# Kernel optimization log

Measured on AMD Instinct MI355X. Metric: run time of the kernel, lower is better.

Reference implementation:

```python
import jax, jax.numpy as jnp
import numpy as np

B, L, D = 4, 512, 768
NUM_SPANS = 4096
MAX_WIDTH = 8
DFF = 4 * D


def setup_inputs() -> dict:
    key = jax.random.key(0)
    k_h, k_s, k_w, k1, k2 = jax.random.split(key, 5)
    h = jax.random.normal(k_h, (B, L, D), dtype=jnp.float32)
    starts = jax.random.randint(k_s, (B, NUM_SPANS), 0, L)
    widths = jax.random.randint(k_w, (B, NUM_SPANS), 1, MAX_WIDTH + 1)
    ends = jnp.minimum(starts + widths - 1, L - 1)
    span_idx = jnp.stack([starts, ends], axis=-1).astype(jnp.int64 if jax.config.jax_enable_x64 else jnp.int32)
    W1 = jax.random.normal(k1, (D, DFF), dtype=jnp.float32) * (1.0 / np.sqrt(D))
    b1 = jnp.zeros((DFF,), dtype=jnp.float32)
    W2 = jax.random.normal(k2, (DFF, D), dtype=jnp.float32) * (1.0 / np.sqrt(DFF))
    b2 = jnp.zeros((D,), dtype=jnp.float32)
    return {"h": h, "span_idx": span_idx, "W1": W1, "b1": b1, "W2": W2, "b2": b2,
            "max_width": MAX_WIDTH}


def reference(h, span_idx, W1, b1, W2, b2, max_width):
    # h: [B, L, D]; span_idx: [B, S, 2] (start, end inclusive)
    Bv, Lv, Dv = h.shape
    starts = span_idx[:, :, 0]                       # [B, S]
    lengths = span_idx[:, :, 1] - starts + 1         # [B, S]
    offsets = jnp.arange(max_width)                  # static bound on span length
    positions = starts[:, :, None] + offsets[None, None, :]      # [B, S, W]
    mask = offsets[None, None, :] < lengths[:, :, None]          # [B, S, W]
    positions = jnp.clip(positions * mask, 0, Lv - 1)
    # indexed gather-reduce (no [B,S,L,D] broadcast): [B, S, W, D]
    gathered = h[jnp.arange(Bv)[:, None, None], positions]
    summed = jnp.sum(gathered * mask[..., None].astype(h.dtype), axis=2)  # [B, S, D]
    span_reps = summed / lengths[..., None].astype(h.dtype)
    # projection: Linear -> ReLU -> (Dropout: identity at eval) -> Linear
    hmid = jax.nn.relu(jnp.einsum('bsd,df->bsf', span_reps, W1) + b1)
    out = jnp.einsum('bsf,fd->bsd', hmid, W2) + b2
    return out
```

## Files before the change

### kernel.cpp

```cpp
#include <hip/hip_runtime.h>
#include <stdint.h>

#define B_DIM 4
#define L_DIM 512
#define D_DIM 768
#define S_DIM 4096
#define DFF_DIM 3072
#define M_DIM (B_DIM * S_DIM)

typedef unsigned short ushort_t;
typedef __attribute__((ext_vector_type(8))) short short8;
typedef __attribute__((ext_vector_type(4))) float floatx4;

__device__ __forceinline__ ushort_t f2bf(float x) {
  unsigned int u = __float_as_uint(x);
  u += 0x7FFFu + ((u >> 16) & 1u);
  return (ushort_t)(u >> 16);
}

__device__ __forceinline__ void load_lds16(const ushort_t* g, ushort_t* lds) {
  __builtin_amdgcn_global_load_lds(
      (const __attribute__((address_space(1))) unsigned int*)g,
      (__attribute__((address_space(3))) unsigned int*)lds, 16, 0, 0);
}

__global__ __launch_bounds__(256)
void transpose_bf16(const float* __restrict__ in, ushort_t* __restrict__ out,
                    int K, int N) {
  __shared__ float tile[32][33];
  const int k0 = blockIdx.x * 32;
  const int n0 = blockIdx.y * 32;
  const int tx = threadIdx.x & 31;
  const int ty = threadIdx.x >> 5;
#pragma unroll
  for (int r = 0; r < 32; r += 8)
    tile[ty + r][tx] = in[(long)(k0 + ty + r) * N + n0 + tx];
  __syncthreads();
#pragma unroll
  for (int r = 0; r < 32; r += 8)
    out[(long)(n0 + ty + r) * K + k0 + tx] = f2bf(tile[tx][ty + r]);
}

__global__ __launch_bounds__(256)
void span_reps(const float* __restrict__ h, const int* __restrict__ span_idx,
               ushort_t* __restrict__ A) {
  const int span = blockIdx.x;
  const int b = span >> 12;
  const int tid = threadIdx.x;
  const int start = span_idx[span * 2 + 0];
  const int end   = span_idx[span * 2 + 1];
  const float inv = 1.0f / (float)(end - start + 1);
  const float* hb = h + ((long)b * L_DIM + start) * D_DIM;
  float a0 = 0.f, a1 = 0.f, a2 = 0.f;
  for (int p = start; p <= end; ++p) {
    a0 += hb[tid];
    a1 += hb[tid + 256];
    a2 += hb[tid + 512];
    hb += D_DIM;
  }
  ushort_t* o = A + (long)span * D_DIM;
  o[tid]       = f2bf(a0 * inv);
  o[tid + 256] = f2bf(a1 * inv);
  o[tid + 512] = f2bf(a2 * inv);
}

template <int MODE>
__global__ __launch_bounds__(256)
void gemm_bt(const ushort_t* __restrict__ A, const ushort_t* __restrict__ Bt,
             const float* __restrict__ bias, void* __restrict__ Cv,
             int M, int N, int K) {
  __shared__ ushort_t As[128 * 32];
  __shared__ ushort_t Bs[128 * 32];

  const int tid  = threadIdx.x;
  const int lane = tid & 63;
  const int wave = tid >> 6;
  const int l16  = lane & 15;
  const int quad = lane >> 4;

  const int bm = blockIdx.x;
  const int bn = blockIdx.y;

  const int wm = (wave & 1) * 64;
  const int wn = (wave >> 1) * 64;

  floatx4 acc[4][4];
#pragma unroll
  for (int i = 0; i < 4; ++i)
#pragma unroll
    for (int j = 0; j < 4; ++j)
      acc[i][j] = (floatx4)0.0f;

  const int s0 = tid, s1 = tid + 256;
  const ushort_t* gA0 = A + (long)(bm * 128 + (s0 >> 2)) * K + (s0 & 3) * 8;
  const ushort_t* gA1 = A + (long)(bm * 128 + (s1 >> 2)) * K + (s1 & 3) * 8;
  const ushort_t* gB0 = Bt + (long)(bn * 128 + (s0 >> 2)) * K + (s0 & 3) * 8;
  const ushort_t* gB1 = Bt + (long)(bn * 128 + (s1 >> 2)) * K + (s1 & 3) * 8;
  ushort_t* lA0 = As + s0 * 8;
  ushort_t* lA1 = As + s1 * 8;
  ushort_t* lB0 = Bs + s0 * 8;
  ushort_t* lB1 = Bs + s1 * 8;

  for (int k0 = 0; k0 < K; k0 += 32) {
    load_lds16(gA0, lA0);
    load_lds16(gA1, lA1);
    load_lds16(gB0, lB0);
    load_lds16(gB1, lB1);
    gA0 += 32; gA1 += 32; gB0 += 32; gB1 += 32;
    __syncthreads();

    short8 af[4], bf[4];
#pragma unroll
    for (int i = 0; i < 4; ++i)
      af[i] = *(const short8*)(As + (wm + i * 16 + l16) * 32 + quad * 8);
#pragma unroll
    for (int j = 0; j < 4; ++j)
      bf[j] = *(const short8*)(Bs + (wn + j * 16 + l16) * 32 + quad * 8);
#pragma unroll
    for (int i = 0; i < 4; ++i)
#pragma unroll
      for (int j = 0; j < 4; ++j)
        acc[i][j] = __builtin_amdgcn_mfma_f32_16x16x32_bf16(af[i], bf[j], acc[i][j], 0, 0, 0);
    __syncthreads();
  }

#pragma unroll
  for (int i = 0; i < 4; ++i) {
#pragma unroll
    for (int j = 0; j < 4; ++j) {
      const int col = bn * 128 + wn + j * 16 + l16;
      const float bv = bias[col];
      const int row0 = bm * 128 + wm + i * 16 + quad * 4;
#pragma unroll
      for (int r = 0; r < 4; ++r) {
        float v = acc[i][j][r] + bv;
        if (MODE == 0) {
          v = v > 0.0f ? v : 0.0f;
          ((ushort_t*)Cv)[(long)(row0 + r) * N + col] = f2bf(v);
        } else {
          ((float*)Cv)[(long)(row0 + r) * N + col] = v;
        }
      }
    }
  }
}

extern "C" void kernel_launch(void* const* d_in, const int* in_sizes, int n_in,
                              void* d_out, int out_size, void* d_ws, size_t ws_size,
                              hipStream_t stream) {
  const float* h        = (const float*)d_in[0];
  const int*   span_idx = (const int*)d_in[1];
  const float* W1       = (const float*)d_in[2];
  const float* b1       = (const float*)d_in[3];
  const float* W2       = (const float*)d_in[4];
  const float* b2       = (const float*)d_in[5];
  float* out = (float*)d_out;

  ushort_t* A   = (ushort_t*)d_ws;
  ushort_t* W1T = A + (size_t)M_DIM * D_DIM;
  ushort_t* W2T = W1T + (size_t)DFF_DIM * D_DIM;
  ushort_t* Hm  = W2T + (size_t)D_DIM * DFF_DIM;

  transpose_bf16<<<dim3(D_DIM / 32, DFF_DIM / 32), 256, 0, stream>>>(W1, W1T, D_DIM, DFF_DIM);
  transpose_bf16<<<dim3(DFF_DIM / 32, D_DIM / 32), 256, 0, stream>>>(W2, W2T, DFF_DIM, D_DIM);

  span_reps<<<M_DIM, 256, 0, stream>>>(h, span_idx, A);

  gemm_bt<0><<<dim3(M_DIM / 128, DFF_DIM / 128), 256, 0, stream>>>(
      A, W1T, b1, Hm, M_DIM, DFF_DIM, D_DIM);

  gemm_bt<1><<<dim3(M_DIM / 128, D_DIM / 128), 256, 0, stream>>>(
      Hm, W2T, b2, out, M_DIM, D_DIM, DFF_DIM);
}
```

Measured before the change: 315.5 us.

## Double-buffer GEMM LDS tiles, swap grid order, one wave per span

The GEMM kernel now double-buffers its A/B LDS tiles, issuing the next k-slice's global-to-LDS loads before computing on the current slice, and keeps one barrier per iteration instead of two. The grid axes are swapped so consecutive blocks walk along N for a fixed M tile, which is meant to improve L2 reuse of the A rows. The span-averaging kernel assigns one wave per span with 12 columns per lane, cutting the block count by four. The aim is to hide load latency and lower launch and barrier overhead, at the cost of doubled LDS use. There is a risk that the async LDS loads are not waited for correctly with only a single barrier per iteration.

```diff
diff --git a/kernel.cpp b/kernel.cpp
--- a/kernel.cpp
+++ b/kernel.cpp
@@ -44,24 +44,25 @@
 __global__ __launch_bounds__(256)
 void span_reps(const float* __restrict__ h, const int* __restrict__ span_idx,
                ushort_t* __restrict__ A) {
-  const int span = blockIdx.x;
+  const int wave = threadIdx.x >> 6;
+  const int lane = threadIdx.x & 63;
+  const int span = blockIdx.x * 4 + wave;
   const int b = span >> 12;
-  const int tid = threadIdx.x;
   const int start = span_idx[span * 2 + 0];
   const int end   = span_idx[span * 2 + 1];
   const float inv = 1.0f / (float)(end - start + 1);
-  const float* hb = h + ((long)b * L_DIM + start) * D_DIM;
-  float a0 = 0.f, a1 = 0.f, a2 = 0.f;
+  const float* hb = h + ((long)b * L_DIM + start) * D_DIM + lane;
+  float a[12];
+#pragma unroll
+  for (int c = 0; c < 12; ++c) a[c] = 0.0f;
   for (int p = start; p <= end; ++p) {
-    a0 += hb[tid];
-    a1 += hb[tid + 256];
-    a2 += hb[tid + 512];
+#pragma unroll
+    for (int c = 0; c < 12; ++c) a[c] += hb[c * 64];
     hb += D_DIM;
   }
-  ushort_t* o = A + (long)span * D_DIM;
-  o[tid]       = f2bf(a0 * inv);
-  o[tid + 256] = f2bf(a1 * inv);
-  o[tid + 512] = f2bf(a2 * inv);
+  ushort_t* o = A + (long)span * D_DIM + lane;
+#pragma unroll
+  for (int c = 0; c < 12; ++c) o[c * 64] = f2bf(a[c] * inv);
 }
 
 template <int MODE>
@@ -69,8 +70,8 @@
 void gemm_bt(const ushort_t* __restrict__ A, const ushort_t* __restrict__ Bt,
              const float* __restrict__ bias, void* __restrict__ Cv,
              int M, int N, int K) {
-  __shared__ ushort_t As[128 * 32];
-  __shared__ ushort_t Bs[128 * 32];
+  __shared__ ushort_t As[2][128 * 32];
+  __shared__ ushort_t Bs[2][128 * 32];
 
   const int tid  = threadIdx.x;
   const int lane = tid & 63;
@@ -78,8 +79,8 @@
   const int l16  = lane & 15;
   const int quad = lane >> 4;
 
-  const int bm = blockIdx.x;
-  const int bn = blockIdx.y;
+  const int bn = blockIdx.x;
+  const int bm = blockIdx.y;
 
   const int wm = (wave & 1) * 64;
   const int wn = (wave >> 1) * 64;
@@ -96,32 +97,39 @@
   const ushort_t* gA1 = A + (long)(bm * 128 + (s1 >> 2)) * K + (s1 & 3) * 8;
   const ushort_t* gB0 = Bt + (long)(bn * 128 + (s0 >> 2)) * K + (s0 & 3) * 8;
   const ushort_t* gB1 = Bt + (long)(bn * 128 + (s1 >> 2)) * K + (s1 & 3) * 8;
-  ushort_t* lA0 = As + s0 * 8;
-  ushort_t* lA1 = As + s1 * 8;
-  ushort_t* lB0 = Bs + s0 * 8;
-  ushort_t* lB1 = Bs + s1 * 8;
 
-  for (int k0 = 0; k0 < K; k0 += 32) {
-    load_lds16(gA0, lA0);
-    load_lds16(gA1, lA1);
-    load_lds16(gB0, lB0);
-    load_lds16(gB1, lB1);
-    gA0 += 32; gA1 += 32; gB0 += 32; gB1 += 32;
+  const int nk = K >> 5;
+
+  load_lds16(gA0, &As[0][0] + s0 * 8);
+  load_lds16(gA1, &As[0][0] + s1 * 8);
+  load_lds16(gB0, &Bs[0][0] + s0 * 8);
+  load_lds16(gB1, &Bs[0][0] + s1 * 8);
+
+  for (int k = 0; k < nk; ++k) {
+    const int cur = k & 1;
+    const int nxt = cur ^ 1;
     __syncthreads();
+
+    if (k + 1 < nk) {
+      const int off = (k + 1) * 32;
+      load_lds16(gA0 + off, &As[nxt][0] + s0 * 8);
+      load_lds16(gA1 + off, &As[nxt][0] + s1 * 8);
+      load_lds16(gB0 + off, &Bs[nxt][0] + s0 * 8);
+      load_lds16(gB1 + off, &Bs[nxt][0] + s1 * 8);
+    }
 
     short8 af[4], bf[4];
 #pragma unroll
     for (int i = 0; i < 4; ++i)
-      af[i] = *(const short8*)(As + (wm + i * 16 + l16) * 32 + quad * 8);
+      af[i] = *(const short8*)(&As[cur][0] + (wm + i * 16 + l16) * 32 + quad * 8);
 #pragma unroll
     for (int j = 0; j < 4; ++j)
-      bf[j] = *(const short8*)(Bs + (wn + j * 16 + l16) * 32 + quad * 8);
+      bf[j] = *(const short8*)(&Bs[cur][0] + (wn + j * 16 + l16) * 32 + quad * 8);
 #pragma unroll
     for (int i = 0; i < 4; ++i)
 #pragma unroll
       for (int j = 0; j < 4; ++j)
         acc[i][j] = __builtin_amdgcn_mfma_f32_16x16x32_bf16(af[i], bf[j], acc[i][j], 0, 0, 0);
-    __syncthreads();
   }
 
 #pragma unroll
@@ -164,11 +172,11 @@
   transpose_bf16<<<dim3(D_DIM / 32, DFF_DIM / 32), 256, 0, stream>>>(W1, W1T, D_DIM, DFF_DIM);
   transpose_bf16<<<dim3(DFF_DIM / 32, D_DIM / 32), 256, 0, stream>>>(W2, W2T, DFF_DIM, D_DIM);
 
-  span_reps<<<M_DIM, 256, 0, stream>>>(h, span_idx, A);
+  span_reps<<<M_DIM / 4, 256, 0, stream>>>(h, span_idx, A);
 
-  gemm_bt<0><<<dim3(M_DIM / 128, DFF_DIM / 128), 256, 0, stream>>>(
+  gemm_bt<0><<<dim3(DFF_DIM / 128, M_DIM / 128), 256, 0, stream>>>(
       A, W1T, b1, Hm, M_DIM, DFF_DIM, D_DIM);
 
-  gemm_bt<1><<<dim3(M_DIM / 128, D_DIM / 128), 256, 0, stream>>>(
+  gemm_bt<1><<<dim3(D_DIM / 128, M_DIM / 128), 256, 0, stream>>>(
       Hm, W2T, b2, out, M_DIM, D_DIM, DFF_DIM);
 }
```

New measurement: 315.1 us. No clear change (-0.1%).
